# Kernel optimization log

Hardware: AMD Instinct MI355X
Metric: run time of the kernel (lower is better)

## Reference

```python
import jax, jax.numpy as jnp
import numpy as np

NUM_HEADS = 16
KEY_SIZE = 64
D_MODEL = 1024


def setup_inputs() -> dict:
    key = jax.random.key(0)
    ks = jax.random.split(key, 9)
    B, S = 2, 2048
    HK = NUM_HEADS * KEY_SIZE
    s = 1.0 / np.sqrt(D_MODEL)
    return {
        "x": jax.random.normal(ks[0], (B, S, D_MODEL), dtype=jnp.float32),
        "Wq": jax.random.normal(ks[1], (D_MODEL, HK), dtype=jnp.float32) * s,
        "bq": jax.random.normal(ks[2], (HK,), dtype=jnp.float32) * 0.02,
        "Wk": jax.random.normal(ks[3], (D_MODEL, HK), dtype=jnp.float32) * s,
        "bk": jax.random.normal(ks[4], (HK,), dtype=jnp.float32) * 0.02,
        "Wv": jax.random.normal(ks[5], (D_MODEL, HK), dtype=jnp.float32) * s,
        "bv": jax.random.normal(ks[6], (HK,), dtype=jnp.float32) * 0.02,
        "Wo": jax.random.normal(ks[7], (HK, D_MODEL), dtype=jnp.float32) * s,
        "bo": jax.random.normal(ks[8], (D_MODEL,), dtype=jnp.float32) * 0.02,
    }


def reference(x, Wq, bq, Wk, bk, Wv, bv, Wo, bo):
    B, S, _ = x.shape
    H, K = NUM_HEADS, KEY_SIZE
    # QKV projections -> (B, H, S, K)
    def proj(W, b):
        return (x @ W + b).reshape(B, S, H, K).transpose(0, 2, 1, 3)
    q = proj(Wq, bq)
    k = proj(Wk, bk)
    v = proj(Wv, bv)
    scale = jnp.sqrt(jnp.float32(K))
    scores = jnp.einsum('bhsk,bhtk->bhst', q, k) / scale  # (B,H,S,S)
    attn = jax.nn.softmax(scores, axis=-1)
    out = jnp.einsum('bhst,bhtk->bhsk', attn, v)  # (B,H,S,K)
    out = out.transpose(0, 2, 1, 3).reshape(B, S, H * K)
    return out @ Wo + bo
```

## Files before the change

kernel.cpp:

```cpp
#include <hip/hip_runtime.h>


#define NH 16
#define KS 64
#define DM 1024
#define BB 2
#define SS 2048
#define NT (BB*SS)
#define HKD 1024
#define L2E 1.44269504088896340736f

typedef __attribute__((ext_vector_type(4))) float floatx4;
typedef __attribute__((ext_vector_type(8))) short short8;

#define BAR() asm volatile("s_barrier" ::: "memory")

__device__ __forceinline__ unsigned short f2b(float f) {
  unsigned u = __builtin_bit_cast(unsigned, f);
  u = (u + 0x7fffu + ((u >> 16) & 1u)) >> 16;
  return (unsigned short)u;
}

__device__ __forceinline__ floatx4 mfma16(short8 a, short8 b, floatx4 c) {
  return __builtin_amdgcn_mfma_f32_16x16x32_bf16(a, b, c, 0, 0, 0);
}

__device__ __forceinline__ void async16(const void* g, void* l) {
  __builtin_amdgcn_global_load_lds(
      (const __attribute__((address_space(1))) unsigned int*)g,
      (__attribute__((address_space(3))) unsigned int*)l, 16, 0, 0);
}

__global__ __launch_bounds__(256) void prep_kernel(
    const float* __restrict__ x,
    const float* __restrict__ Wq, const float* __restrict__ Wk,
    const float* __restrict__ Wv, const float* __restrict__ Wo,
    unsigned short* __restrict__ xb,
    unsigned short* __restrict__ wqt, unsigned short* __restrict__ wkt,
    unsigned short* __restrict__ wvt, unsigned short* __restrict__ wot) {
  int bid = blockIdx.x;
  if (bid < NT * DM / 1024) {
    int i = (bid * 256 + threadIdx.x) * 4;
    float4 v = *(const float4*)(x + i);
    ushort4 o;
    o.x = f2b(v.x); o.y = f2b(v.y); o.z = f2b(v.z); o.w = f2b(v.w);
    *(ushort4*)(xb + i) = o;
    return;
  }
  int b2 = bid - NT * DM / 1024;
  int z = b2 >> 8;
  const float* W; unsigned short* Wt;
  if (z == 0)      { W = Wq; Wt = wqt; }
  else if (z == 1) { W = Wk; Wt = wkt; }
  else if (z == 2) { W = Wv; Wt = wvt; }
  else             { W = Wo; Wt = wot; }
  __shared__ __align__(16) unsigned short tile[64][80];
  int k0 = (b2 & 15) * 64, n0 = ((b2 >> 4) & 15) * 64;
  int t = threadIdx.x;
  int c0 = (t & 15) * 4, r = t >> 4;
  #pragma unroll
  for (int p = 0; p < 4; ++p) {
    int rr = r + p * 16;
    float4 v = *(const float4*)(W + (k0 + rr) * DM + n0 + c0);
    tile[c0 + 0][rr] = f2b(v.x);
    tile[c0 + 1][rr] = f2b(v.y);
    tile[c0 + 2][rr] = f2b(v.z);
    tile[c0 + 3][rr] = f2b(v.w);
  }
  __syncthreads();
  int cc0 = (t & 7) * 8, rn = t >> 3;
  #pragma unroll
  for (int p = 0; p < 2; ++p) {
    int nn = rn + p * 32;
    *(short8*)(Wt + (n0 + nn) * DM + k0 + cc0) = *(const short8*)(&tile[nn][cc0]);
  }
}

__global__ __launch_bounds__(256) void gemm_qkv_kernel(
    const unsigned short* __restrict__ xb,
    const unsigned short* __restrict__ wqt, const unsigned short* __restrict__ wkt,
    const unsigned short* __restrict__ wvt,
    const float* __restrict__ bq, const float* __restrict__ bk, const float* __restrict__ bv,
    unsigned short* __restrict__ qb, unsigned short* __restrict__ kbuf,
    unsigned short* __restrict__ vt) {
  __shared__ __align__(16) unsigned short smem[18432];
  const unsigned short* Bt; const float* bias; float scale; int zid = blockIdx.z;
  if (zid == 0)      { Bt = wqt; bias = bq; scale = 0.125f * L2E; }
  else if (zid == 1) { Bt = wkt; bias = bk; scale = 1.0f; }
  else               { Bt = wvt; bias = bv; scale = 1.0f; }
  int m0 = blockIdx.x * 128, n0 = blockIdx.y * 128;
  int t = threadIdx.x, w = t >> 6, lane = t & 63, cl = lane & 15, quad = lane >> 4;
  int wr = (w >> 1) * 64, wc = (w & 1) * 64;
  floatx4 acc[4][4];
  #pragma unroll
  for (int i = 0; i < 4; ++i)
    #pragma unroll
    for (int j = 0; j < 4; ++j)
      acc[i][j] = floatx4{0.f, 0.f, 0.f, 0.f};

  auto stage = [&](int kc, int buf) {
    #pragma unroll
    for (int i = 0; i < 2; ++i) {
      int c = i * 256 + t;
      int row = c >> 2, col = (c & 3) ^ (row & 3);
      async16(xb + (m0 + row) * DM + kc * 32 + col * 8, &smem[buf * 4096 + c * 8]);
      async16(Bt + (n0 + row) * DM + kc * 32 + col * 8, &smem[8192 + buf * 4096 + c * 8]);
    }
  };
  stage(0, 0);
  stage(1, 1);

  for (int kc = 0; kc < DM / 32; ++kc) {
    int cur = kc & 1;
    if (kc < DM / 32 - 1) asm volatile("s_waitcnt vmcnt(4)" ::: "memory");
    else                  asm volatile("s_waitcnt vmcnt(0)" ::: "memory");
    BAR();
    const unsigned short* Ac = &smem[cur * 4096];
    const unsigned short* Bc = &smem[8192 + cur * 4096];
    short8 a[4], b[4];
    #pragma unroll
    for (int i = 0; i < 4; ++i)
      a[i] = *(const short8*)&Ac[(wr + i * 16 + cl) * 32 + ((quad ^ (cl & 3)) * 8)];
    #pragma unroll
    for (int j = 0; j < 4; ++j)
      b[j] = *(const short8*)&Bc[(wc + j * 16 + cl) * 32 + ((quad ^ (cl & 3)) * 8)];
    #pragma unroll
    for (int i = 0; i < 4; ++i)
      #pragma unroll
      for (int j = 0; j < 4; ++j)
        acc[i][j] = mfma16(a[i], b[j], acc[i][j]);
    BAR();
    if (kc + 2 < DM / 32) stage(kc + 2, cur);
  }
  __syncthreads();

  int h = (n0 + wc) >> 6;
  if (zid < 2) {
    unsigned short* dst = (zid == 0) ? qb : kbuf;
    #pragma unroll
    for (int j = 0; j < 4; ++j) {
      float bj = bias[n0 + wc + j * 16 + cl];
      int kd = j * 16 + cl;
      #pragma unroll
      for (int i = 0; i < 4; ++i)
        #pragma unroll
        for (int r = 0; r < 4; ++r) {
          int token = m0 + wr + i * 16 + quad * 4 + r;
          int bz = token >> 11, s = token & (SS - 1);
          float val = (acc[i][j][r] + bj) * scale;
          dst[(((bz * NH + h) * SS + s) << 6) + kd] = f2b(val);
        }
    }
  } else {
    unsigned short* tr = &smem[w * 4608];
    #pragma unroll
    for (int j = 0; j < 4; ++j) {
      float bj = bias[n0 + wc + j * 16 + cl];
      #pragma unroll
      for (int i = 0; i < 4; ++i) {
        unsigned short b0 = f2b(acc[i][j][0] + bj), b1 = f2b(acc[i][j][1] + bj);
        unsigned short b2 = f2b(acc[i][j][2] + bj), b3 = f2b(acc[i][j][3] + bj);
        uint2 pk;
        pk.x = (unsigned)b0 | ((unsigned)b1 << 16);
        pk.y = (unsigned)b2 | ((unsigned)b3 << 16);
        *(uint2*)&tr[(j * 16 + cl) * 72 + i * 16 + quad * 4] = pk;
      }
    }
    asm volatile("s_waitcnt lgkmcnt(0)" ::: "memory");
    int tokbase = m0 + wr;
    int bz = tokbase >> 11, s0 = tokbase & (SS - 1);
    unsigned short* vdst = vt + (((bz * NH + h) * KS) * SS) + s0;
    #pragma unroll
    for (int p = 0; p < 8; ++p) {
      int row = p * 8 + (lane >> 3);
      int tk = (lane & 7) * 8;
      short8 vv = *(const short8*)&tr[row * 72 + tk];
      *(short8*)(vdst + row * SS + tk) = vv;
    }
  }
}

__global__ __launch_bounds__(512) void attn_kernel(
    const unsigned short* __restrict__ Q, const unsigned short* __restrict__ Kb,
    const unsigned short* __restrict__ Vt, unsigned short* __restrict__ AO) {
  __shared__ __align__(16) unsigned short smem[40960];
  int t = threadIdx.x, w = t >> 6, lane = t & 63, cl = lane & 15, quad = lane >> 4;
  int clm = cl & 7, cl3 = cl & 3, cl2 = cl >> 2;
  int id = blockIdx.x + (SS / 256) * (blockIdx.y + NH * blockIdx.z);
  int c = id & 7, k = id >> 3;
  int head_lin = c + 8 * (k & 3);
  int qx = k >> 2;
  int h = head_lin & (NH - 1), bz = head_lin >> 4;
  int bh = bz * NH + h;
  int slice = w & 3, part = w >> 2;
  int q0 = qx * 256 + slice * 64;
  const unsigned short* Qp = Q + (bh * SS + q0) * KS;
  const unsigned short* Kp = Kb + bh * SS * KS;
  const unsigned short* Vp = Vt + bh * KS * SS;
  unsigned short* p_w = smem + 24576 + w * 2048;

  short8 qa[4][2];
  #pragma unroll
  for (int qt = 0; qt < 4; ++qt)
    #pragma unroll
    for (int cc = 0; cc < 2; ++cc)
      qa[qt][cc] = *(const short8*)(Qp + (qt * 16 + cl) * KS + cc * 32 + quad * 8);

  short8 ones;
  #pragma unroll
  for (int j = 0; j < 8; ++j) ones[j] = (short)0x3f80;

  floatx4 lacc[4];
  floatx4 oa[4][4];
  #pragma unroll
  for (int qt = 0; qt < 4; ++qt) {
    lacc[qt] = floatx4{0.f, 0.f, 0.f, 0.f};
    #pragma unroll
    for (int j = 0; j < 4; ++j) oa[qt][j] = floatx4{0.f, 0.f, 0.f, 0.f};
  }

  int st = t >> 8, lt = t & 255;
  int krow = lt >> 3, kcol = (lt & 7) ^ (krow & 7);
  int vd = lt >> 2, vcol = ((lt & 3) ^ (vd & 3) ^ ((vd >> 2) & 3)) & 3;
  auto stage = [&](int it, int buf) {
    async16(Kp + (st * 1024 + it * 32 + krow) * KS + kcol * 8,
            &smem[(st * 3 + buf) * 2048 + lt * 8]);
    async16(Vp + vd * SS + st * 1024 + it * 32 + vcol * 8,
            &smem[12288 + (st * 3 + buf) * 2048 + lt * 8]);
  };
  stage(0, 0);
  stage(1, 1);

  const int NIT = 1024 / 32;
  int cur = 0;
  for (int it = 0; it < NIT; ++it) {
    if (it < NIT - 1) asm volatile("s_waitcnt vmcnt(2)" ::: "memory");
    else              asm volatile("s_waitcnt vmcnt(0)" ::: "memory");
    BAR();
    if (it + 2 < NIT) {
      int sb = (cur >= 1) ? cur - 1 : 2;
      stage(it + 2, sb);
    }
    const unsigned short* Kc = &smem[(part * 3 + cur) * 2048];
    const unsigned short* Vc = &smem[12288 + (part * 3 + cur) * 2048];

    floatx4 s[4][2];
    __builtin_amdgcn_s_setprio(1);
    #pragma unroll
    for (int kt = 0; kt < 2; ++kt) {
      short8 kb0 = *(const short8*)&Kc[(kt * 16 + cl) * 64 + ((quad ^ clm) * 8)];
      short8 kb1 = *(const short8*)&Kc[(kt * 16 + cl) * 64 + (((4 + quad) ^ clm) * 8)];
      #pragma unroll
      for (int qt = 0; qt < 4; ++qt) {
        floatx4 z = {0.f, 0.f, 0.f, 0.f};
        s[qt][kt] = mfma16(kb1, qa[qt][1], mfma16(kb0, qa[qt][0], z));
      }
    }
    __builtin_amdgcn_s_setprio(0);
    #pragma unroll
    for (int qt = 0; qt < 4; ++qt)
      #pragma unroll
      for (int kt = 0; kt < 2; ++kt) {
        unsigned u[4];
        #pragma unroll
        for (int r = 0; r < 4; ++r)
          u[r] = __builtin_bit_cast(unsigned, __builtin_amdgcn_exp2f(s[qt][kt][r]));
        uint2 pk;
        pk.x = __builtin_amdgcn_perm(u[1], u[0], 0x07060302);
        pk.y = __builtin_amdgcn_perm(u[3], u[2], 0x07060302);
        int blk = ((kt * 2 + (quad >> 1)) ^ cl3 ^ cl2) & 3;
        int off = qt * 512 + cl * 32 + blk * 8 + (quad & 1) * 4;
        *(uint2*)(p_w + off) = pk;
      }
    asm volatile("s_waitcnt lgkmcnt(0)" ::: "memory");
    short8 pa[4];
    __builtin_amdgcn_s_setprio(1);
    #pragma unroll
    for (int qt = 0; qt < 4; ++qt) {
      pa[qt] = *(const short8*)(p_w + qt * 512 + cl * 32 + (((quad ^ cl3 ^ cl2) & 3) * 8));
      lacc[qt] = mfma16(ones, pa[qt], lacc[qt]);
    }
    #pragma unroll
    for (int j = 0; j < 4; ++j) {
      short8 vb = *(const short8*)&Vc[(j * 16 + cl) * 32 + (((quad ^ cl3 ^ cl2) & 3) * 8)];
      #pragma unroll
      for (int qt = 0; qt < 4; ++qt)
        oa[qt][j] = mfma16(vb, pa[qt], oa[qt][j]);
    }
    __builtin_amdgcn_s_setprio(0);
    cur = (cur == 2) ? 0 : cur + 1;
  }

  __syncthreads();
  float* red = (float*)smem;
  float* base = red + slice * 4352;
  if (part == 1) {
    #pragma unroll
    for (int qt = 0; qt < 4; ++qt)
      #pragma unroll
      for (int j = 0; j < 4; ++j)
        *(floatx4*)(base + (((qt * 4 + j) * 64 + lane) << 2)) = oa[qt][j];
    #pragma unroll
    for (int qt = 0; qt < 4; ++qt)
      base[4096 + lane * 4 + qt] = lacc[qt][0];
  }
  __syncthreads();
  if (part == 0) {
    #pragma unroll
    for (int qt = 0; qt < 4; ++qt)
      #pragma unroll
      for (int j = 0; j < 4; ++j)
        oa[qt][j] += *(const floatx4*)(base + (((qt * 4 + j) * 64 + lane) << 2));
    float lsum[4];
    #pragma unroll
    for (int qt = 0; qt < 4; ++qt)
      lsum[qt] = lacc[qt][0] + base[4096 + lane * 4 + qt];
    #pragma unroll
    for (int qt = 0; qt < 4; ++qt) {
      float inv = 1.0f / lsum[qt];
      unsigned short* aop = AO + (bz * SS + q0 + qt * 16 + cl) * DM + h * KS + quad * 4;
      #pragma unroll
      for (int j = 0; j < 4; ++j) {
        unsigned short b0 = f2b(oa[qt][j][0] * inv), b1 = f2b(oa[qt][j][1] * inv);
        unsigned short b2 = f2b(oa[qt][j][2] * inv), b3 = f2b(oa[qt][j][3] * inv);
        uint2 pk;
        pk.x = (unsigned)b0 | ((unsigned)b1 << 16);
        pk.y = (unsigned)b2 | ((unsigned)b3 << 16);
        *(uint2*)(aop + j * 16) = pk;
      }
    }
  }
}

__global__ __launch_bounds__(256) void gemm_out_kernel(
    const unsigned short* __restrict__ ao, const unsigned short* __restrict__ wot,
    const float* __restrict__ bo, float* __restrict__ out) {
  __shared__ __align__(16) unsigned short As[2][8192], Bs[2][2048];
  int m0 = blockIdx.x * 256, n0 = blockIdx.y * 64;
  int t = threadIdx.x, w = t >> 6, lane = t & 63, cl = lane & 15, quad = lane >> 4;
  int wr = w * 64;
  floatx4 acc[4][4];
  #pragma unroll
  for (int i = 0; i < 4; ++i)
    #pragma unroll
    for (int j = 0; j < 4; ++j)
      acc[i][j] = floatx4{0.f, 0.f, 0.f, 0.f};

  auto stage = [&](int kc, int buf) {
    #pragma unroll
    for (int i = 0; i < 4; ++i) {
      int c = i * 256 + t;
      int row = c >> 2, col = (c & 3) ^ (row & 3);
      async16(ao + (m0 + row) * HKD + kc * 32 + col * 8, &As[buf][c * 8]);
    }
    {
      int c = t;
      int row = c >> 2, col = (c & 3) ^ (row & 3);
      async16(wot + (n0 + row) * HKD + kc * 32 + col * 8, &Bs[buf][c * 8]);
    }
  };
  stage(0, 0);
  stage(1, 1);

  for (int kc = 0; kc < HKD / 32; ++kc) {
    int cur = kc & 1;
    if (kc < HKD / 32 - 1) asm volatile("s_waitcnt vmcnt(5)" ::: "memory");
    else                   asm volatile("s_waitcnt vmcnt(0)" ::: "memory");
    BAR();
    short8 a[4], b[4];
    #pragma unroll
    for (int i = 0; i < 4; ++i)
      a[i] = *(const short8*)&As[cur][(wr + i * 16 + cl) * 32 + ((quad ^ (cl & 3)) * 8)];
    #pragma unroll
    for (int j = 0; j < 4; ++j)
      b[j] = *(const short8*)&Bs[cur][(j * 16 + cl) * 32 + ((quad ^ (cl & 3)) * 8)];
    #pragma unroll
    for (int i = 0; i < 4; ++i)
      #pragma unroll
      for (int j = 0; j < 4; ++j)
        acc[i][j] = mfma16(a[i], b[j], acc[i][j]);
    BAR();
    if (kc + 2 < HKD / 32) stage(kc + 2, cur);
  }
  #pragma unroll
  for (int j = 0; j < 4; ++j) {
    float bj = bo[n0 + j * 16 + cl];
    #pragma unroll
    for (int i = 0; i < 4; ++i)
      #pragma unroll
      for (int r = 0; r < 4; ++r) {
        int token = m0 + wr + i * 16 + quad * 4 + r;
        out[token * DM + n0 + j * 16 + cl] = acc[i][j][r] + bj;
      }
  }
}

extern "C" void kernel_launch(void* const* d_in, const int* in_sizes, int n_in,
                              void* d_out, int out_size, void* d_ws, size_t ws_size,
                              hipStream_t stream) {
  const float* x  = (const float*)d_in[0];
  const float* Wq = (const float*)d_in[1];
  const float* bq = (const float*)d_in[2];
  const float* Wk = (const float*)d_in[3];
  const float* bk = (const float*)d_in[4];
  const float* Wv = (const float*)d_in[5];
  const float* bv = (const float*)d_in[6];
  const float* Wo = (const float*)d_in[7];
  const float* bo = (const float*)d_in[8];
  float* out = (float*)d_out;
  char* ws = (char*)d_ws;
  unsigned short* xb  = (unsigned short*)(ws);
  unsigned short* wqt = (unsigned short*)(ws + (8ull  << 20));
  unsigned short* wkt = (unsigned short*)(ws + (10ull << 20));
  unsigned short* wvt = (unsigned short*)(ws + (12ull << 20));
  unsigned short* wot = (unsigned short*)(ws + (14ull << 20));
  unsigned short* qb  = (unsigned short*)(ws + (16ull << 20));
  unsigned short* kbf = (unsigned short*)(ws + (24ull << 20));
  unsigned short* vt  = (unsigned short*)(ws + (40ull << 20));
  unsigned short* ao  = (unsigned short*)(ws + (48ull << 20));

  hipLaunchKernelGGL(prep_kernel, dim3(NT * DM / 1024 + 1024), dim3(256), 0, stream,
                     x, Wq, Wk, Wv, Wo, xb, wqt, wkt, wvt, wot);
  hipLaunchKernelGGL(gemm_qkv_kernel, dim3(NT / 128, HKD / 128, 3), dim3(256), 0, stream,
                     xb, wqt, wkt, wvt, bq, bk, bv, qb, kbf, vt);
  hipLaunchKernelGGL(attn_kernel, dim3(SS / 256, NH, BB), dim3(512), 0, stream, qb, kbf, vt, ao);
  hipLaunchKernelGGL(gemm_out_kernel, dim3(NT / 256, DM / 64), dim3(256), 0, stream, ao, wot, bo, out);
}
```

Measured before the change: 195.9 us.

## Software-pipeline attention loop so PV of previous tile overlaps QK exp

Restructures the attention main loop so each iteration computes QK^T for the current K tile while doing the P·V and row-sum MFMAs for the previous tile's probabilities, with an epilogue for the last tile. The K/V staging ring grows from three to four buffers, raising LDS use, so the V tile from the previous iteration stays valid while new tiles are prefetched. The aim is to let the exp/pack VALU work and the MFMA work interleave instead of running back-to-back, at the cost of more registers and LDS.

Result: no change. 196.1 us (+0.1%).

```diff
diff --git a/kernel.cpp b/kernel.cpp
--- a/kernel.cpp
+++ b/kernel.cpp
@@ -183,7 +183,7 @@
 __global__ __launch_bounds__(512) void attn_kernel(
     const unsigned short* __restrict__ Q, const unsigned short* __restrict__ Kb,
     const unsigned short* __restrict__ Vt, unsigned short* __restrict__ AO) {
-  __shared__ __align__(16) unsigned short smem[40960];
+  __shared__ __align__(16) unsigned short smem[49152];
   int t = threadIdx.x, w = t >> 6, lane = t & 63, cl = lane & 15, quad = lane >> 4;
   int clm = cl & 7, cl3 = cl & 3, cl2 = cl >> 2;
   int id = blockIdx.x + (SS / 256) * (blockIdx.y + NH * blockIdx.z);
@@ -197,7 +197,7 @@
   const unsigned short* Qp = Q + (bh * SS + q0) * KS;
   const unsigned short* Kp = Kb + bh * SS * KS;
   const unsigned short* Vp = Vt + bh * KS * SS;
-  unsigned short* p_w = smem + 24576 + w * 2048;
+  unsigned short* p_w = smem + 32768 + w * 2048;
 
   short8 qa[4][2];
   #pragma unroll
@@ -222,41 +222,62 @@
   int st = t >> 8, lt = t & 255;
   int krow = lt >> 3, kcol = (lt & 7) ^ (krow & 7);
   int vd = lt >> 2, vcol = ((lt & 3) ^ (vd & 3) ^ ((vd >> 2) & 3)) & 3;
-  auto stage = [&](int it, int buf) {
-    async16(Kp + (st * 1024 + it * 32 + krow) * KS + kcol * 8,
-            &smem[(st * 3 + buf) * 2048 + lt * 8]);
-    async16(Vp + vd * SS + st * 1024 + it * 32 + vcol * 8,
-            &smem[12288 + (st * 3 + buf) * 2048 + lt * 8]);
+  auto stage = [&](int it2, int buf) {
+    async16(Kp + (st * 1024 + it2 * 32 + krow) * KS + kcol * 8,
+            &smem[(st * 4 + buf) * 2048 + lt * 8]);
+    async16(Vp + vd * SS + st * 1024 + it2 * 32 + vcol * 8,
+            &smem[16384 + (st * 4 + buf) * 2048 + lt * 8]);
   };
   stage(0, 0);
   stage(1, 1);
 
   const int NIT = 1024 / 32;
-  int cur = 0;
   for (int it = 0; it < NIT; ++it) {
     if (it < NIT - 1) asm volatile("s_waitcnt vmcnt(2)" ::: "memory");
     else              asm volatile("s_waitcnt vmcnt(0)" ::: "memory");
     BAR();
-    if (it + 2 < NIT) {
-      int sb = (cur >= 1) ? cur - 1 : 2;
-      stage(it + 2, sb);
-    }
-    const unsigned short* Kc = &smem[(part * 3 + cur) * 2048];
-    const unsigned short* Vc = &smem[12288 + (part * 3 + cur) * 2048];
+    if (it + 2 < NIT) stage(it + 2, (it + 2) & 3);
+    const unsigned short* Kc = &smem[(part * 4 + (it & 3)) * 2048];
+
+    short8 kb[2][2];
+    #pragma unroll
+    for (int kt = 0; kt < 2; ++kt) {
+      kb[kt][0] = *(const short8*)&Kc[(kt * 16 + cl) * 64 + ((quad ^ clm) * 8)];
+      kb[kt][1] = *(const short8*)&Kc[(kt * 16 + cl) * 64 + (((4 + quad) ^ clm) * 8)];
+    }
+    short8 vb[4], pa[4];
+    if (it > 0) {
+      const unsigned short* Vc = &smem[16384 + (part * 4 + ((it - 1) & 3)) * 2048];
+      #pragma unroll
+      for (int j = 0; j < 4; ++j)
+        vb[j] = *(const short8*)&Vc[(j * 16 + cl) * 32 + (((quad ^ cl3 ^ cl2) & 3) * 8)];
+      #pragma unroll
+      for (int qt = 0; qt < 4; ++qt)
+        pa[qt] = *(const short8*)(p_w + qt * 512 + cl * 32 + (((quad ^ cl3 ^ cl2) & 3) * 8));
+    }
+    asm volatile("s_waitcnt lgkmcnt(0)" ::: "memory");
 
     floatx4 s[4][2];
     __builtin_amdgcn_s_setprio(1);
     #pragma unroll
-    for (int kt = 0; kt < 2; ++kt) {
-      short8 kb0 = *(const short8*)&Kc[(kt * 16 + cl) * 64 + ((quad ^ clm) * 8)];
-      short8 kb1 = *(const short8*)&Kc[(kt * 16 + cl) * 64 + (((4 + quad) ^ clm) * 8)];
+    for (int kt = 0; kt < 2; ++kt)
       #pragma unroll
       for (int qt = 0; qt < 4; ++qt) {
         floatx4 z = {0.f, 0.f, 0.f, 0.f};
-        s[qt][kt] = mfma16(kb1, qa[qt][1], mfma16(kb0, qa[qt][0], z));
+        s[qt][kt] = mfma16(kb[kt][1], qa[qt][1], mfma16(kb[kt][0], qa[qt][0], z));
       }
+    if (it > 0) {
+      #pragma unroll
+      for (int qt = 0; qt < 4; ++qt)
+        lacc[qt] = mfma16(ones, pa[qt], lacc[qt]);
+      #pragma unroll
+      for (int j = 0; j < 4; ++j)
+        #pragma unroll
+        for (int qt = 0; qt < 4; ++qt)
+          oa[qt][j] = mfma16(vb[j], pa[qt], oa[qt][j]);
     }
     __builtin_amdgcn_s_setprio(0);
+
     #pragma unroll
     for (int qt = 0; qt < 4; ++qt)
       #pragma unroll
@@ -272,23 +293,26 @@
         int off = qt * 512 + cl * 32 + blk * 8 + (quad & 1) * 4;
         *(uint2*)(p_w + off) = pk;
       }
+  }
+
+  {
+    const unsigned short* Vc = &smem[16384 + (part * 4 + ((NIT - 1) & 3)) * 2048];
+    short8 vb[4], pa[4];
+    #pragma unroll
+    for (int j = 0; j < 4; ++j)
+      vb[j] = *(const short8*)&Vc[(j * 16 + cl) * 32 + (((quad ^ cl3 ^ cl2) & 3) * 8)];
+    #pragma unroll
+    for (int qt = 0; qt < 4; ++qt)
+      pa[qt] = *(const short8*)(p_w + qt * 512 + cl * 32 + (((quad ^ cl3 ^ cl2) & 3) * 8));
     asm volatile("s_waitcnt lgkmcnt(0)" ::: "memory");
-    short8 pa[4];
-    __builtin_amdgcn_s_setprio(1);
-    #pragma unroll
-    for (int qt = 0; qt < 4; ++qt) {
-      pa[qt] = *(const short8*)(p_w + qt * 512 + cl * 32 + (((quad ^ cl3 ^ cl2) & 3) * 8));
+    #pragma unroll
+    for (int qt = 0; qt < 4; ++qt)
       lacc[qt] = mfma16(ones, pa[qt], lacc[qt]);
-    }
-    #pragma unroll
-    for (int j = 0; j < 4; ++j) {
-      short8 vb = *(const short8*)&Vc[(j * 16 + cl) * 32 + (((quad ^ cl3 ^ cl2) & 3) * 8)];
+    #pragma unroll
+    for (int j = 0; j < 4; ++j)
       #pragma unroll
       for (int qt = 0; qt < 4; ++qt)
-        oa[qt][j] = mfma16(vb, pa[qt], oa[qt][j]);
-    }
-    __builtin_amdgcn_s_setprio(0);
-    cur = (cur == 2) ? 0 : cur + 1;
+        oa[qt][j] = mfma16(vb[j], pa[qt], oa[qt][j]);
   }
 
   __syncthreads();
```

## Process two KV tiles per iteration with 4-deep ring and interleaved QK/PV

Applied to the files above, without the earlier changes.

Grows the K/V shared-memory ring from 3 to 4 buffers and handles two 32-key tiles per loop iteration. All K and V fragments for both tiles are loaded into registers before a second barrier, after which the next two tiles are staged. The QK MFMAs of the second tile are interleaved with the exp/pack and PV work of the first, so MFMA work overlaps the exp and LDS traffic, and barriers per key drop by half. The costs are more LDS (96KB total), higher register pressure from holding both tiles' fragments, and a second barrier per iteration. The per-wave P buffer is reused by both tiles and relies on the lgkmcnt wait ordering between its write and read.

New measurement: 195.5 us. About the same (-0.2%).

```diff
diff --git a/kernel.cpp b/kernel.cpp
--- a/kernel.cpp
+++ b/kernel.cpp
@@ -183,7 +183,7 @@
 __global__ __launch_bounds__(512) void attn_kernel(
     const unsigned short* __restrict__ Q, const unsigned short* __restrict__ Kb,
     const unsigned short* __restrict__ Vt, unsigned short* __restrict__ AO) {
-  __shared__ __align__(16) unsigned short smem[40960];
+  __shared__ __align__(16) unsigned short smem[49152];
   int t = threadIdx.x, w = t >> 6, lane = t & 63, cl = lane & 15, quad = lane >> 4;
   int clm = cl & 7, cl3 = cl & 3, cl2 = cl >> 2;
   int id = blockIdx.x + (SS / 256) * (blockIdx.y + NH * blockIdx.z);
@@ -197,7 +197,7 @@
   const unsigned short* Qp = Q + (bh * SS + q0) * KS;
   const unsigned short* Kp = Kb + bh * SS * KS;
   const unsigned short* Vp = Vt + bh * KS * SS;
-  unsigned short* p_w = smem + 24576 + w * 2048;
+  unsigned short* p_w = smem + 32768 + w * 2048;
 
   short8 qa[4][2];
   #pragma unroll
@@ -222,41 +222,25 @@
   int st = t >> 8, lt = t & 255;
   int krow = lt >> 3, kcol = (lt & 7) ^ (krow & 7);
   int vd = lt >> 2, vcol = ((lt & 3) ^ (vd & 3) ^ ((vd >> 2) & 3)) & 3;
-  auto stage = [&](int it, int buf) {
-    async16(Kp + (st * 1024 + it * 32 + krow) * KS + kcol * 8,
-            &smem[(st * 3 + buf) * 2048 + lt * 8]);
-    async16(Vp + vd * SS + st * 1024 + it * 32 + vcol * 8,
-            &smem[12288 + (st * 3 + buf) * 2048 + lt * 8]);
-  };
-  stage(0, 0);
-  stage(1, 1);
-
-  const int NIT = 1024 / 32;
-  int cur = 0;
-  for (int it = 0; it < NIT; ++it) {
-    if (it < NIT - 1) asm volatile("s_waitcnt vmcnt(2)" ::: "memory");
-    else              asm volatile("s_waitcnt vmcnt(0)" ::: "memory");
-    BAR();
-    if (it + 2 < NIT) {
-      int sb = (cur >= 1) ? cur - 1 : 2;
-      stage(it + 2, sb);
-    }
-    const unsigned short* Kc = &smem[(part * 3 + cur) * 2048];
-    const unsigned short* Vc = &smem[12288 + (part * 3 + cur) * 2048];
-
-    floatx4 s[4][2];
-    __builtin_amdgcn_s_setprio(1);
-    #pragma unroll
-    for (int kt = 0; kt < 2; ++kt) {
-      short8 kb0 = *(const short8*)&Kc[(kt * 16 + cl) * 64 + ((quad ^ clm) * 8)];
-      short8 kb1 = *(const short8*)&Kc[(kt * 16 + cl) * 64 + (((4 + quad) ^ clm) * 8)];
+  auto stage = [&](int tile) {
+    int buf = tile & 3;
+    async16(Kp + (st * 1024 + tile * 32 + krow) * KS + kcol * 8,
+            &smem[(st * 4 + buf) * 2048 + lt * 8]);
+    async16(Vp + vd * SS + st * 1024 + tile * 32 + vcol * 8,
+            &smem[16384 + (st * 4 + buf) * 2048 + lt * 8]);
+  };
+  stage(0); stage(1); stage(2); stage(3);
+
+  auto qk_tile = [&](const short8 kb[2][2], floatx4 s[4][2]) {
+    #pragma unroll
+    for (int kt = 0; kt < 2; ++kt)
       #pragma unroll
       for (int qt = 0; qt < 4; ++qt) {
         floatx4 z = {0.f, 0.f, 0.f, 0.f};
-        s[qt][kt] = mfma16(kb1, qa[qt][1], mfma16(kb0, qa[qt][0], z));
+        s[qt][kt] = mfma16(kb[kt][1], qa[qt][1], mfma16(kb[kt][0], qa[qt][0], z));
       }
-    }
-    __builtin_amdgcn_s_setprio(0);
+  };
+  auto exp_pack_write = [&](const floatx4 s[4][2]) {
     #pragma unroll
     for (int qt = 0; qt < 4; ++qt)
       #pragma unroll
@@ -272,23 +256,66 @@
         int off = qt * 512 + cl * 32 + blk * 8 + (quad & 1) * 4;
         *(uint2*)(p_w + off) = pk;
       }
+  };
+  auto pv_tile = [&](const short8 vb[4]) {
+    short8 pa[4];
+    #pragma unroll
+    for (int qt = 0; qt < 4; ++qt)
+      pa[qt] = *(const short8*)(p_w + qt * 512 + cl * 32 + (((quad ^ cl3 ^ cl2) & 3) * 8));
     asm volatile("s_waitcnt lgkmcnt(0)" ::: "memory");
-    short8 pa[4];
+    #pragma unroll
+    for (int qt = 0; qt < 4; ++qt)
+      lacc[qt] = mfma16(ones, pa[qt], lacc[qt]);
+    #pragma unroll
+    for (int j = 0; j < 4; ++j)
+      #pragma unroll
+      for (int qt = 0; qt < 4; ++qt)
+        oa[qt][j] = mfma16(vb[j], pa[qt], oa[qt][j]);
+  };
+
+  const int NP = 16;
+  for (int p = 0; p < NP; ++p) {
+    int a = 2 * p, b = 2 * p + 1;
+    if (p < NP - 1) asm volatile("s_waitcnt vmcnt(4)" ::: "memory");
+    else            asm volatile("s_waitcnt vmcnt(0)" ::: "memory");
+    BAR();
+    const unsigned short* Ka = &smem[(part * 4 + (a & 3)) * 2048];
+    const unsigned short* Kb_ = &smem[(part * 4 + (b & 3)) * 2048];
+    const unsigned short* Va = &smem[16384 + (part * 4 + (a & 3)) * 2048];
+    const unsigned short* Vb_ = &smem[16384 + (part * 4 + (b & 3)) * 2048];
+    short8 kba[2][2], kbb[2][2], vba[4], vbb[4];
+    #pragma unroll
+    for (int kt = 0; kt < 2; ++kt) {
+      kba[kt][0] = *(const short8*)&Ka[(kt * 16 + cl) * 64 + ((quad ^ clm) * 8)];
+      kba[kt][1] = *(const short8*)&Ka[(kt * 16 + cl) * 64 + (((4 + quad) ^ clm) * 8)];
+      kbb[kt][0] = *(const short8*)&Kb_[(kt * 16 + cl) * 64 + ((quad ^ clm) * 8)];
+      kbb[kt][1] = *(const short8*)&Kb_[(kt * 16 + cl) * 64 + (((4 + quad) ^ clm) * 8)];
+    }
+    #pragma unroll
+    for (int j = 0; j < 4; ++j) {
+      vba[j] = *(const short8*)&Va[(j * 16 + cl) * 32 + (((quad ^ cl3 ^ cl2) & 3) * 8)];
+      vbb[j] = *(const short8*)&Vb_[(j * 16 + cl) * 32 + (((quad ^ cl3 ^ cl2) & 3) * 8)];
+    }
+    asm volatile("s_waitcnt lgkmcnt(0)" ::: "memory");
+    BAR();
+    if (p < NP - 2) { stage(a + 4); stage(b + 4); }
+
+    floatx4 s[4][2];
     __builtin_amdgcn_s_setprio(1);
-    #pragma unroll
-    for (int qt = 0; qt < 4; ++qt) {
-      pa[qt] = *(const short8*)(p_w + qt * 512 + cl * 32 + (((quad ^ cl3 ^ cl2) & 3) * 8));
-      lacc[qt] = mfma16(ones, pa[qt], lacc[qt]);
-    }
-    #pragma unroll
-    for (int j = 0; j < 4; ++j) {
-      short8 vb = *(const short8*)&Vc[(j * 16 + cl) * 32 + (((quad ^ cl3 ^ cl2) & 3) * 8)];
-      #pragma unroll
-      for (int qt = 0; qt < 4; ++qt)
-        oa[qt][j] = mfma16(vb, pa[qt], oa[qt][j]);
-    }
+    qk_tile(kba, s);
     __builtin_amdgcn_s_setprio(0);
-    cur = (cur == 2) ? 0 : cur + 1;
+    exp_pack_write(s);
+    floatx4 s2[4][2];
+    __builtin_amdgcn_s_setprio(1);
+    qk_tile(kbb, s2);
+    __builtin_amdgcn_s_setprio(0);
+    __builtin_amdgcn_s_setprio(1);
+    pv_tile(vba);
+    __builtin_amdgcn_s_setprio(0);
+    exp_pack_write(s2);
+    __builtin_amdgcn_s_setprio(1);
+    pv_tile(vbb);
+    __builtin_amdgcn_s_setprio(0);
   }
 
   __syncthreads();
```

## Fuse all stages into one cooperative persistent kernel with grid syncs

Applied to the files above, without the earlier changes.

Merges the conversion, QKV projection, attention and output projection into a single cooperative kernel of 256 blocks, separated by grid-wide syncs, with the old four-kernel path kept as a fallback. GEMM stages are retiled to 128x128 per block with 8 waves of 64x32 each. This aims to remove launch gaps and tail effects between kernels, at the cost of grid-sync overhead and only one block per CU, which reduces latency hiding.

Measured after the change: 397.2 us. 103% more time.

```diff
diff --git a/kernel.cpp b/kernel.cpp
--- a/kernel.cpp
+++ b/kernel.cpp
@@ -1,4 +1,7 @@
 #include <hip/hip_runtime.h>
+#include <hip/hip_cooperative_groups.h>
+
+namespace cg = cooperative_groups;
 
 
 #define NH 16
@@ -29,6 +32,357 @@
   __builtin_amdgcn_global_load_lds(
       (const __attribute__((address_space(1))) unsigned int*)g,
       (__attribute__((address_space(3))) unsigned int*)l, 16, 0, 0);
+}
+
+__global__ __launch_bounds__(512) void mha_fused_kernel(
+    const float* __restrict__ x,
+    const float* __restrict__ Wq, const float* __restrict__ Wk,
+    const float* __restrict__ Wv, const float* __restrict__ Wo,
+    const float* __restrict__ bq, const float* __restrict__ bk,
+    const float* __restrict__ bv, const float* __restrict__ bo,
+    unsigned short* __restrict__ xb,
+    unsigned short* __restrict__ wqt, unsigned short* __restrict__ wkt,
+    unsigned short* __restrict__ wvt, unsigned short* __restrict__ wot,
+    unsigned short* __restrict__ qb, unsigned short* __restrict__ kbf,
+    unsigned short* __restrict__ vt, unsigned short* __restrict__ ao,
+    float* __restrict__ out) {
+  __shared__ __align__(16) unsigned short smem[40960];
+  int wg = blockIdx.x, t = threadIdx.x;
+  int w = t >> 6, lane = t & 63, cl = lane & 15, quad = lane >> 4;
+
+  {
+    #pragma unroll
+    for (int r = 0; r < 8; ++r) {
+      int i = ((r * 256 + wg) * 512 + t) * 4;
+      float4 v = *(const float4*)(x + i);
+      ushort4 o;
+      o.x = f2b(v.x); o.y = f2b(v.y); o.z = f2b(v.z); o.w = f2b(v.w);
+      *(ushort4*)(xb + i) = o;
+    }
+    int half = t >> 8, tid = t & 255;
+    unsigned short (*tile)[80] = (unsigned short(*)[80])(smem + half * 5120);
+    for (int pp = 0; pp < 2; ++pp) {
+      int gt = wg * 4 + pp * 2 + half;
+      int z = gt >> 8, b2 = gt & 255;
+      const float* W = (z == 0) ? Wq : (z == 1) ? Wk : (z == 2) ? Wv : Wo;
+      unsigned short* Wt = (z == 0) ? wqt : (z == 1) ? wkt : (z == 2) ? wvt : wot;
+      int k0 = (b2 & 15) * 64, n0 = (b2 >> 4) * 64;
+      int c0 = (tid & 15) * 4, rr0 = tid >> 4;
+      #pragma unroll
+      for (int p = 0; p < 4; ++p) {
+        int rr = rr0 + p * 16;
+        float4 v = *(const float4*)(W + (k0 + rr) * DM + n0 + c0);
+        tile[c0 + 0][rr] = f2b(v.x);
+        tile[c0 + 1][rr] = f2b(v.y);
+        tile[c0 + 2][rr] = f2b(v.z);
+        tile[c0 + 3][rr] = f2b(v.w);
+      }
+      __syncthreads();
+      int cc0 = (tid & 7) * 8, rn = tid >> 3;
+      #pragma unroll
+      for (int p = 0; p < 2; ++p) {
+        int nn = rn + p * 32;
+        *(short8*)(Wt + (n0 + nn) * DM + k0 + cc0) = *(const short8*)(&tile[nn][cc0]);
+      }
+      __syncthreads();
+    }
+  }
+  __threadfence();
+  cg::this_grid().sync();
+
+  {
+    int m0 = (wg & 31) * 128, n0 = ((wg >> 5) & 7) * 128;
+    int wr = (w >> 2) * 64, wc = (w & 3) * 32;
+    int srow = t >> 2, scol = (t & 3) ^ (srow & 3);
+    for (int z = 0; z < 3; ++z) {
+      const unsigned short* Bt = (z == 0) ? wqt : (z == 1) ? wkt : wvt;
+      const float* bias = (z == 0) ? bq : (z == 1) ? bk : bv;
+      float scale = (z == 0) ? 0.125f * L2E : 1.0f;
+      floatx4 acc[4][2];
+      #pragma unroll
+      for (int i = 0; i < 4; ++i)
+        #pragma unroll
+        for (int j = 0; j < 2; ++j)
+          acc[i][j] = floatx4{0.f, 0.f, 0.f, 0.f};
+      auto stg = [&](int kc, int buf) {
+        async16(xb + (m0 + srow) * DM + kc * 32 + scol * 8, &smem[buf * 4096 + t * 8]);
+        async16(Bt + (n0 + srow) * DM + kc * 32 + scol * 8, &smem[8192 + buf * 4096 + t * 8]);
+      };
+      stg(0, 0);
+      stg(1, 1);
+      for (int kc = 0; kc < DM / 32; ++kc) {
+        int cur = kc & 1;
+        if (kc < DM / 32 - 1) asm volatile("s_waitcnt vmcnt(2)" ::: "memory");
+        else                  asm volatile("s_waitcnt vmcnt(0)" ::: "memory");
+        BAR();
+        const unsigned short* Ac = &smem[cur * 4096];
+        const unsigned short* Bc = &smem[8192 + cur * 4096];
+        short8 a[4], b[2];
+        #pragma unroll
+        for (int i = 0; i < 4; ++i)
+          a[i] = *(const short8*)&Ac[(wr + i * 16 + cl) * 32 + ((quad ^ (cl & 3)) * 8)];
+        #pragma unroll
+        for (int j = 0; j < 2; ++j)
+          b[j] = *(const short8*)&Bc[(wc + j * 16 + cl) * 32 + ((quad ^ (cl & 3)) * 8)];
+        #pragma unroll
+        for (int i = 0; i < 4; ++i)
+          #pragma unroll
+          for (int j = 0; j < 2; ++j)
+            acc[i][j] = mfma16(a[i], b[j], acc[i][j]);
+        BAR();
+        if (kc + 2 < DM / 32) stg(kc + 2, cur);
+      }
+      int h = (n0 + wc) >> 6;
+      int kdb = (n0 + wc) & 63;
+      if (z < 2) {
+        unsigned short* dst = (z == 0) ? qb : kbf;
+        #pragma unroll
+        for (int j = 0; j < 2; ++j) {
+          float bj = bias[n0 + wc + j * 16 + cl];
+          int kd = kdb + j * 16 + cl;
+          #pragma unroll
+          for (int i = 0; i < 4; ++i)
+            #pragma unroll
+            for (int r = 0; r < 4; ++r) {
+              int token = m0 + wr + i * 16 + quad * 4 + r;
+              int bz = token >> 11, s = token & (SS - 1);
+              float val = (acc[i][j][r] + bj) * scale;
+              dst[(((bz * NH + h) * SS + s) << 6) + kd] = f2b(val);
+            }
+        }
+      } else {
+        unsigned short* tr = &smem[16384 + w * 2304];
+        #pragma unroll
+        for (int j = 0; j < 2; ++j) {
+          float bj = bias[n0 + wc + j * 16 + cl];
+          #pragma unroll
+          for (int i = 0; i < 4; ++i) {
+            unsigned short b0 = f2b(acc[i][j][0] + bj), b1 = f2b(acc[i][j][1] + bj);
+            unsigned short b2 = f2b(acc[i][j][2] + bj), b3 = f2b(acc[i][j][3] + bj);
+            uint2 pk;
+            pk.x = (unsigned)b0 | ((unsigned)b1 << 16);
+            pk.y = (unsigned)b2 | ((unsigned)b3 << 16);
+            *(uint2*)&tr[(j * 16 + cl) * 72 + i * 16 + quad * 4] = pk;
+          }
+        }
+        asm volatile("s_waitcnt lgkmcnt(0)" ::: "memory");
+        int tokbase = m0 + wr;
+        int bz = tokbase >> 11, s0 = tokbase & (SS - 1);
+        unsigned short* vdst = vt + ((bz * NH + h) * KS + kdb) * SS + s0;
+        #pragma unroll
+        for (int p = 0; p < 4; ++p) {
+          int row = p * 8 + (lane >> 3);
+          int tk = (lane & 7) * 8;
+          short8 vv = *(const short8*)&tr[row * 72 + tk];
+          *(short8*)(vdst + row * SS + tk) = vv;
+        }
+      }
+      __syncthreads();
+    }
+  }
+  __threadfence();
+  cg::this_grid().sync();
+
+  {
+    int clm = cl & 7, cl3 = cl & 3, cl2 = cl >> 2;
+    int id = wg;
+    int c = id & 7, k = id >> 3;
+    int head_lin = c + 8 * (k & 3);
+    int qx = k >> 2;
+    int h = head_lin & (NH - 1), bz = head_lin >> 4;
+    int bh = bz * NH + h;
+    int slice = w & 3, part = w >> 2;
+    int q0 = qx * 256 + slice * 64;
+    const unsigned short* Qp = qb + (bh * SS + q0) * KS;
+    const unsigned short* Kp = kbf + bh * SS * KS;
+    const unsigned short* Vp = vt + bh * KS * SS;
+    unsigned short* p_w = smem + 24576 + w * 2048;
+
+    short8 qa[4][2];
+    #pragma unroll
+    for (int qt = 0; qt < 4; ++qt)
+      #pragma unroll
+      for (int cc = 0; cc < 2; ++cc)
+        qa[qt][cc] = *(const short8*)(Qp + (qt * 16 + cl) * KS + cc * 32 + quad * 8);
+
+    short8 ones;
+    #pragma unroll
+    for (int j = 0; j < 8; ++j) ones[j] = (short)0x3f80;
+
+    floatx4 lacc[4];
+    floatx4 oa[4][4];
+    #pragma unroll
+    for (int qt = 0; qt < 4; ++qt) {
+      lacc[qt] = floatx4{0.f, 0.f, 0.f, 0.f};
+      #pragma unroll
+      for (int j = 0; j < 4; ++j) oa[qt][j] = floatx4{0.f, 0.f, 0.f, 0.f};
+    }
+
+    int st = t >> 8, lt = t & 255;
+    int krow = lt >> 3, kcol = (lt & 7) ^ (krow & 7);
+    int vd = lt >> 2, vcol = ((lt & 3) ^ (vd & 3) ^ ((vd >> 2) & 3)) & 3;
+    auto stage = [&](int it, int buf) {
+      async16(Kp + (st * 1024 + it * 32 + krow) * KS + kcol * 8,
+              &smem[(st * 3 + buf) * 2048 + lt * 8]);
+      async16(Vp + vd * SS + st * 1024 + it * 32 + vcol * 8,
+              &smem[12288 + (st * 3 + buf) * 2048 + lt * 8]);
+    };
+    stage(0, 0);
+    stage(1, 1);
+
+    const int NIT = 1024 / 32;
+    int cur = 0;
+    for (int it = 0; it < NIT; ++it) {
+      if (it < NIT - 1) asm volatile("s_waitcnt vmcnt(2)" ::: "memory");
+      else              asm volatile("s_waitcnt vmcnt(0)" ::: "memory");
+      BAR();
+      if (it + 2 < NIT) {
+        int sb = (cur >= 1) ? cur - 1 : 2;
+        stage(it + 2, sb);
+      }
+      const unsigned short* Kc = &smem[(part * 3 + cur) * 2048];
+      const unsigned short* Vc = &smem[12288 + (part * 3 + cur) * 2048];
+
+      floatx4 s[4][2];
+      __builtin_amdgcn_s_setprio(1);
+      #pragma unroll
+      for (int kt = 0; kt < 2; ++kt) {
+        short8 kb0 = *(const short8*)&Kc[(kt * 16 + cl) * 64 + ((quad ^ clm) * 8)];
+        short8 kb1 = *(const short8*)&Kc[(kt * 16 + cl) * 64 + (((4 + quad) ^ clm) * 8)];
+        #pragma unroll
+        for (int qt = 0; qt < 4; ++qt) {
+          floatx4 z = {0.f, 0.f, 0.f, 0.f};
+          s[qt][kt] = mfma16(kb1, qa[qt][1], mfma16(kb0, qa[qt][0], z));
+        }
+      }
+      __builtin_amdgcn_s_setprio(0);
+      #pragma unroll
+      for (int qt = 0; qt < 4; ++qt)
+        #pragma unroll
+        for (int kt = 0; kt < 2; ++kt) {
+          unsigned u[4];
+          #pragma unroll
+          for (int r = 0; r < 4; ++r)
+            u[r] = __builtin_bit_cast(unsigned, __builtin_amdgcn_exp2f(s[qt][kt][r]));
+          uint2 pk;
+          pk.x = __builtin_amdgcn_perm(u[1], u[0], 0x07060302);
+          pk.y = __builtin_amdgcn_perm(u[3], u[2], 0x07060302);
+          int blk = ((kt * 2 + (quad >> 1)) ^ cl3 ^ cl2) & 3;
+          int off = qt * 512 + cl * 32 + blk * 8 + (quad & 1) * 4;
+          *(uint2*)(p_w + off) = pk;
+        }
+      asm volatile("s_waitcnt lgkmcnt(0)" ::: "memory");
+      short8 pa[4];
+      __builtin_amdgcn_s_setprio(1);
+      #pragma unroll
+      for (int qt = 0; qt < 4; ++qt) {
+        pa[qt] = *(const short8*)(p_w + qt * 512 + cl * 32 + (((quad ^ cl3 ^ cl2) & 3) * 8));
+        lacc[qt] = mfma16(ones, pa[qt], lacc[qt]);
+      }
+      #pragma unroll
+      for (int j = 0; j < 4; ++j) {
+        short8 vb = *(const short8*)&Vc[(j * 16 + cl) * 32 + (((quad ^ cl3 ^ cl2) & 3) * 8)];
+        #pragma unroll
+        for (int qt = 0; qt < 4; ++qt)
+          oa[qt][j] = mfma16(vb, pa[qt], oa[qt][j]);
+      }
+      __builtin_amdgcn_s_setprio(0);
+      cur = (cur == 2) ? 0 : cur + 1;
+    }
+
+    __syncthreads();
+    float* red = (float*)smem;
+    float* base = red + slice * 4352;
+    if (part == 1) {
+      #pragma unroll
+      for (int qt = 0; qt < 4; ++qt)
+        #pragma unroll
+        for (int j = 0; j < 4; ++j)
+          *(floatx4*)(base + (((qt * 4 + j) * 64 + lane) << 2)) = oa[qt][j];
+      #pragma unroll
+      for (int qt = 0; qt < 4; ++qt)
+        base[4096 + lane * 4 + qt] = lacc[qt][0];
+    }
+    __syncthreads();
+    if (part == 0) {
+      #pragma unroll
+      for (int qt = 0; qt < 4; ++qt)
+        #pragma unroll
+        for (int j = 0; j < 4; ++j)
+          oa[qt][j] += *(const floatx4*)(base + (((qt * 4 + j) * 64 + lane) << 2));
+      float lsum[4];
+      #pragma unroll
+      for (int qt = 0; qt < 4; ++qt)
+        lsum[qt] = lacc[qt][0] + base[4096 + lane * 4 + qt];
+      #pragma unroll
+      for (int qt = 0; qt < 4; ++qt) {
+        float inv = 1.0f / lsum[qt];
+        unsigned short* aop = ao + (bz * SS + q0 + qt * 16 + cl) * DM + h * KS + quad * 4;
+        #pragma unroll
+        for (int j = 0; j < 4; ++j) {
+          unsigned short b0 = f2b(oa[qt][j][0] * inv), b1 = f2b(oa[qt][j][1] * inv);
+          unsigned short b2 = f2b(oa[qt][j][2] * inv), b3 = f2b(oa[qt][j][3] * inv);
+          uint2 pk;
+          pk.x = (unsigned)b0 | ((unsigned)b1 << 16);
+          pk.y = (unsigned)b2 | ((unsigned)b3 << 16);
+          *(uint2*)(aop + j * 16) = pk;
+        }
+      }
+    }
+  }
+  __threadfence();
+  cg::this_grid().sync();
+
+  {
+    int m0 = (wg & 31) * 128, n0 = (wg >> 5) * 128;
+    int wr = (w >> 2) * 64, wc = (w & 3) * 32;
+    int srow = t >> 2, scol = (t & 3) ^ (srow & 3);
+    floatx4 acc[4][2];
+    #pragma unroll
+    for (int i = 0; i < 4; ++i)
+      #pragma unroll
+      for (int j = 0; j < 2; ++j)
+        acc[i][j] = floatx4{0.f, 0.f, 0.f, 0.f};
+    auto stg = [&](int kc, int buf) {
+      async16(ao + (m0 + srow) * HKD + kc * 32 + scol * 8, &smem[buf * 4096 + t * 8]);
+      async16(wot + (n0 + srow) * HKD + kc * 32 + scol * 8, &smem[8192 + buf * 4096 + t * 8]);
+    };
+    stg(0, 0);
+    stg(1, 1);
+    for (int kc = 0; kc < HKD / 32; ++kc) {
+      int cur = kc & 1;
+      if (kc < HKD / 32 - 1) asm volatile("s_waitcnt vmcnt(2)" ::: "memory");
+      else                   asm volatile("s_waitcnt vmcnt(0)" ::: "memory");
+      BAR();
+      const unsigned short* Ac = &smem[cur * 4096];
+      const unsigned short* Bc = &smem[8192 + cur * 4096];
+      short8 a[4], b[2];
+      #pragma unroll
+      for (int i = 0; i < 4; ++i)
+        a[i] = *(const short8*)&Ac[(wr + i * 16 + cl) * 32 + ((quad ^ (cl & 3)) * 8)];
+      #pragma unroll
+      for (int j = 0; j < 2; ++j)
+        b[j] = *(const short8*)&Bc[(wc + j * 16 + cl) * 32 + ((quad ^ (cl & 3)) * 8)];
+      #pragma unroll
+      for (int i = 0; i < 4; ++i)
+        #pragma unroll
+        for (int j = 0; j < 2; ++j)
+          acc[i][j] = mfma16(a[i], b[j], acc[i][j]);
+      BAR();
+      if (kc + 2 < HKD / 32) stg(kc + 2, cur);
+    }
+    #pragma unroll
+    for (int j = 0; j < 2; ++j) {
+      float bj = bo[n0 + wc + j * 16 + cl];
+      #pragma unroll
+      for (int i = 0; i < 4; ++i)
+        #pragma unroll
+        for (int r = 0; r < 4; ++r) {
+          int token = m0 + wr + i * 16 + quad * 4 + r;
+          out[token * DM + n0 + wc + j * 16 + cl] = acc[i][j][r] + bj;
+        }
+    }
+  }
 }
 
 __global__ __launch_bounds__(256) void prep_kernel(
@@ -97,7 +451,6 @@
     #pragma unroll
     for (int j = 0; j < 4; ++j)
       acc[i][j] = floatx4{0.f, 0.f, 0.f, 0.f};
-
   auto stage = [&](int kc, int buf) {
     #pragma unroll
     for (int i = 0; i < 2; ++i) {
@@ -109,7 +462,6 @@
   };
   stage(0, 0);
   stage(1, 1);
-
   for (int kc = 0; kc < DM / 32; ++kc) {
     int cur = kc & 1;
     if (kc < DM / 32 - 1) asm volatile("s_waitcnt vmcnt(4)" ::: "memory");
@@ -133,7 +485,6 @@
     if (kc + 2 < DM / 32) stage(kc + 2, cur);
   }
   __syncthreads();
-
   int h = (n0 + wc) >> 6;
   if (zid < 2) {
     unsigned short* dst = (zid == 0) ? qb : kbuf;
@@ -198,18 +549,15 @@
   const unsigned short* Kp = Kb + bh * SS * KS;
   const unsigned short* Vp = Vt + bh * KS * SS;
   unsigned short* p_w = smem + 24576 + w * 2048;
-
   short8 qa[4][2];
   #pragma unroll
   for (int qt = 0; qt < 4; ++qt)
     #pragma unroll
     for (int cc = 0; cc < 2; ++cc)
       qa[qt][cc] = *(const short8*)(Qp + (qt * 16 + cl) * KS + cc * 32 + quad * 8);
-
   short8 ones;
   #pragma unroll
   for (int j = 0; j < 8; ++j) ones[j] = (short)0x3f80;
-
   floatx4 lacc[4];
   floatx4 oa[4][4];
   #pragma unroll
@@ -218,7 +566,6 @@
     #pragma unroll
     for (int j = 0; j < 4; ++j) oa[qt][j] = floatx4{0.f, 0.f, 0.f, 0.f};
   }
-
   int st = t >> 8, lt = t & 255;
   int krow = lt >> 3, kcol = (lt & 7) ^ (krow & 7);
   int vd = lt >> 2, vcol = ((lt & 3) ^ (vd & 3) ^ ((vd >> 2) & 3)) & 3;
@@ -230,7 +577,6 @@
   };
   stage(0, 0);
   stage(1, 1);
-
   const int NIT = 1024 / 32;
   int cur = 0;
   for (int it = 0; it < NIT; ++it) {
@@ -243,7 +589,6 @@
     }
     const unsigned short* Kc = &smem[(part * 3 + cur) * 2048];
     const unsigned short* Vc = &smem[12288 + (part * 3 + cur) * 2048];
-
     floatx4 s[4][2];
     __builtin_amdgcn_s_setprio(1);
     #pragma unroll
@@ -290,7 +635,6 @@
     __builtin_amdgcn_s_setprio(0);
     cur = (cur == 2) ? 0 : cur + 1;
   }
-
   __syncthreads();
   float* red = (float*)smem;
   float* base = red + slice * 4352;
@@ -345,7 +689,6 @@
     #pragma unroll
     for (int j = 0; j < 4; ++j)
       acc[i][j] = floatx4{0.f, 0.f, 0.f, 0.f};
-
   auto stage = [&](int kc, int buf) {
     #pragma unroll
     for (int i = 0; i < 4; ++i) {
@@ -361,7 +704,6 @@
   };
   stage(0, 0);
   stage(1, 1);
-
   for (int kc = 0; kc < HKD / 32; ++kc) {
     int cur = kc & 1;
     if (kc < HKD / 32 - 1) asm volatile("s_waitcnt vmcnt(5)" ::: "memory");
@@ -419,10 +761,18 @@
   unsigned short* vt  = (unsigned short*)(ws + (40ull << 20));
   unsigned short* ao  = (unsigned short*)(ws + (48ull << 20));
 
-  hipLaunchKernelGGL(prep_kernel, dim3(NT * DM / 1024 + 1024), dim3(256), 0, stream,
-                     x, Wq, Wk, Wv, Wo, xb, wqt, wkt, wvt, wot);
-  hipLaunchKernelGGL(gemm_qkv_kernel, dim3(NT / 128, HKD / 128, 3), dim3(256), 0, stream,
-                     xb, wqt, wkt, wvt, bq, bk, bv, qb, kbf, vt);
-  hipLaunchKernelGGL(attn_kernel, dim3(SS / 256, NH, BB), dim3(512), 0, stream, qb, kbf, vt, ao);
-  hipLaunchKernelGGL(gemm_out_kernel, dim3(NT / 256, DM / 64), dim3(256), 0, stream, ao, wot, bo, out);
-}
+  void* args[] = {(void*)&x, (void*)&Wq, (void*)&Wk, (void*)&Wv, (void*)&Wo,
+                  (void*)&bq, (void*)&bk, (void*)&bv, (void*)&bo,
+                  (void*)&xb, (void*)&wqt, (void*)&wkt, (void*)&wvt, (void*)&wot,
+                  (void*)&qb, (void*)&kbf, (void*)&vt, (void*)&ao, (void*)&out};
+  hipError_t err = hipLaunchCooperativeKernel((void*)mha_fused_kernel,
+                                              dim3(256), dim3(512), args, 0, stream);
+  if (err != hipSuccess) {
+    hipLaunchKernelGGL(prep_kernel, dim3(NT * DM / 1024 + 1024), dim3(256), 0, stream,
+                       x, Wq, Wk, Wv, Wo, xb, wqt, wkt, wvt, wot);
+    hipLaunchKernelGGL(gemm_qkv_kernel, dim3(NT / 128, HKD / 128, 3), dim3(256), 0, stream,
+                       xb, wqt, wkt, wvt, bq, bk, bv, qb, kbf, vt);
+    hipLaunchKernelGGL(attn_kernel, dim3(SS / 256, NH, BB), dim3(512), 0, stream, qb, kbf, vt, ao);
+    hipLaunchKernelGGL(gemm_out_kernel, dim3(NT / 256, DM / 64), dim3(256), 0, stream, ao, wot, bo, out);
+  }
+}
```
